# Kernel optimization log

Hardware: AMD Instinct MI355X
Metric: run time of the kernel (lower is better)

Reference implementation:

```python
import jax, jax.numpy as jnp
import numpy as np

N = 100_000      # nodes
E = 1_600_000    # edges
F_IN = 128       # input features
H = 128          # hidden features
G = 500          # graphs in batch
C = 10           # output classes


def setup_inputs() -> dict:
    key = jax.random.key(0)
    ks = jax.random.split(key, 10)
    x = jax.random.normal(ks[0], (N, F_IN), dtype=jnp.float32)
    edge_index = jax.random.randint(ks[1], (2, E), 0, N, dtype=jnp.int32)
    batch = jnp.sort(jax.random.randint(ks[2], (N,), 0, G, dtype=jnp.int32))
    s1 = 1.0 / np.sqrt(F_IN)
    s2 = 1.0 / np.sqrt(H)
    s3 = 1.0 / np.sqrt(2 * H)
    W1 = jax.random.normal(ks[3], (F_IN, H), jnp.float32) * s1
    W2 = jax.random.normal(ks[4], (H, H), jnp.float32) * s2
    W3 = jax.random.normal(ks[5], (H, H), jnp.float32) * s2
    fc_W = jax.random.normal(ks[6], (2 * H, C), jnp.float32) * s3
    return {
        "x": x, "edge_index": edge_index, "batch": batch,
        "W1": W1, "b1": jnp.zeros((H,), jnp.float32),
        "W2": W2, "b2": jnp.zeros((H,), jnp.float32),
        "W3": W3, "b3": jnp.zeros((H,), jnp.float32),
        "fc_W": fc_W, "fc_b": jnp.zeros((C,), jnp.float32),
    }


def gcn_conv(x, W, b, src, dst, dinv):
    # PyG GCNConv: add self-loops, symmetric norm deg^-1/2 * deg^-1/2,
    # transform then gather-scale-scatter aggregate at dst.
    h = x @ W                                   # [N, H]
    norm = dinv[src] * dinv[dst]                # [E]
    agg = jax.ops.segment_sum(h[src] * norm[:, None], dst, num_segments=N)
    agg = agg + h * (dinv * dinv)[:, None]      # self-loop contribution
    return agg + b


def reference(x, edge_index, batch, W1, b1, W2, b2, W3, b3, fc_W, fc_b):
    src, dst = edge_index[0], edge_index[1]
    # degree (with self-loop) from target counts, as in PyG's gcn_norm
    deg = jax.ops.segment_sum(jnp.ones((E,), x.dtype), dst, num_segments=N) + 1.0
    dinv = jax.lax.rsqrt(deg)

    h = jax.nn.relu(gcn_conv(x, W1, b1, src, dst, dinv))
    h = jax.nn.relu(gcn_conv(h, W2, b2, src, dst, dinv))
    # dropout is identity in eval mode
    h = jax.nn.relu(gcn_conv(h, W3, b3, src, dst, dinv))

    counts = jax.ops.segment_sum(jnp.ones((N,), h.dtype), batch, num_segments=G)
    x_mean = jax.ops.segment_sum(h, batch, num_segments=G) / jnp.maximum(counts, 1.0)[:, None]
    x_max = jax.ops.segment_max(h, batch, num_segments=G)
    pooled = jnp.concatenate([x_mean, x_max], axis=1)   # [G, 2H]
    return pooled @ fc_W + fc_b                          # [G, C]
```

## Files before the change

### kernel.cpp

```cpp
#include <hip/hip_runtime.h>
#include <hip/hip_fp16.h>


typedef _Float16 f16;
typedef f16 f16x8 __attribute__((ext_vector_type(8)));
typedef f16 f16x4 __attribute__((ext_vector_type(4)));
typedef f16 f16x2 __attribute__((ext_vector_type(2)));
typedef float f32x4 __attribute__((ext_vector_type(4)));

#define BIN_BITS 8
#define BINSZ 256
#define CB 256
#define SRC_BITS 17

__global__ __launch_bounds__(256) void prep_count(const float* __restrict__ W1,
                                                  const float* __restrict__ W2,
                                                  const float* __restrict__ W3,
                                                  f16x8* __restrict__ wf,
                                                  const int* __restrict__ dst,
                                                  int* __restrict__ bcnt,
                                                  int ne, int nb, int chunk) {
    int bid = blockIdx.x;
    int t = threadIdx.x;
    if (bid < 24) {
        int layer = bid >> 3;
        const float* W = (layer == 0) ? W1 : (layer == 1 ? W2 : W3);
        int tid2 = (bid & 7) * 256 + t;
        int ch = tid2 >> 10;
        int ct = (tid2 >> 8) & 3;
        int tt = (tid2 >> 6) & 3;
        int l  = tid2 & 63;
        int c  = ch * 64 + ct * 16 + (l & 15);
        int k0 = tt * 32 + ((l >> 4) << 3);
        f16x8 v;
#pragma unroll
        for (int j = 0; j < 8; ++j) v[j] = (f16)W[(size_t)(k0 + j) * 128 + c];
        wf[layer * 2048 + tid2] = v;
        return;
    }
    __shared__ int h[512];
    int b = bid - 24;
    for (int i = t; i < 512; i += 256) h[i] = 0;
    __syncthreads();
    int e0 = b * chunk, e1 = min(ne, e0 + chunk);
    for (int e = e0 + t; e < e1; e += 256)
        atomicAdd(&h[dst[e] >> BIN_BITS], 1);
    __syncthreads();
    for (int i = t; i < nb; i += 256) bcnt[(size_t)b * 512 + i] = h[i];
}

__global__ __launch_bounds__(256) void binscan(int* __restrict__ bcnt,
                                               int* __restrict__ tot, int nb) {
    __shared__ int ws[4];
    int bin = blockIdx.x;
    int t = threadIdx.x;
    int v = bcnt[(size_t)t * 512 + bin];
    int lane = t & 63, wid = t >> 6;
    int sc = v;
#pragma unroll
    for (int off = 1; off < 64; off <<= 1) {
        int u = __shfl_up(sc, off, 64);
        if (lane >= off) sc += u;
    }
    if (lane == 63) ws[wid] = sc;
    __syncthreads();
    if (t == 0) { int r = 0; for (int i = 0; i < 4; ++i) { int x = ws[i]; ws[i] = r; r += x; } }
    __syncthreads();
    int excl = ws[wid] + sc - v;
    bcnt[(size_t)t * 512 + bin] = excl;
    if (t == 255) tot[bin] = excl + v;
}

__global__ __launch_bounds__(512) void s512scan(const int* __restrict__ tot,
                                                int* __restrict__ base,
                                                int* __restrict__ row_ptr,
                                                int nb, int n, int ne) {
    __shared__ int ws[8];
    int t = threadIdx.x;
    int v = (t < nb) ? tot[t] : 0;
    int lane = t & 63, wid = t >> 6;
    int sc = v;
#pragma unroll
    for (int off = 1; off < 64; off <<= 1) {
        int u = __shfl_up(sc, off, 64);
        if (lane >= off) sc += u;
    }
    if (lane == 63) ws[wid] = sc;
    __syncthreads();
    if (t == 0) { int r = 0; for (int i = 0; i < 8; ++i) { int x = ws[i]; ws[i] = r; r += x; } }
    __syncthreads();
    int excl = ws[wid] + sc - v;
    if (t < nb) base[t] = excl;
    if (t == 0) { base[nb] = ne; row_ptr[n] = ne; }
}

__global__ __launch_bounds__(256) void bucket_place(const int* __restrict__ src,
                                                    const int* __restrict__ dst,
                                                    const int* __restrict__ base,
                                                    const int* __restrict__ bcnt,
                                                    unsigned* __restrict__ ebuf,
                                                    int ne, int nb, int chunk) {
    __shared__ int cur[512];
    __shared__ int rel[512];
    int b = blockIdx.x;
    int t = threadIdx.x;
    for (int i = t; i < 512; i += 256) {
        cur[i] = 0;
        rel[i] = (i < nb) ? (base[i] + bcnt[(size_t)b * 512 + i]) : 0;
    }
    __syncthreads();
    int e0 = b * chunk, e1 = min(ne, e0 + chunk);
    for (int e = e0 + t; e < e1; e += 256) {
        int d = dst[e];
        int s = src[e];
        int bin = d >> BIN_BITS;
        int rank = atomicAdd(&cur[bin], 1);
        ebuf[(size_t)rel[bin] + rank] = (unsigned)s | ((unsigned)(d & (BINSZ - 1)) << SRC_BITS);
    }
}

__global__ __launch_bounds__(256) void place_kernel(const unsigned* __restrict__ ebuf,
                                                    const int* __restrict__ base,
                                                    int* __restrict__ row_ptr,
                                                    int* __restrict__ csr,
                                                    float* __restrict__ dinv, int n) {
    __shared__ int hist[BINSZ];
    __shared__ int cur[BINSZ];
    __shared__ int ws[4];
    int bin = blockIdx.x;
    int t = threadIdx.x;
    int node0 = bin << BIN_BITS;
    int ebeg = base[bin], eend = base[bin + 1];
    hist[t] = 0;
    __syncthreads();
    for (int p = ebeg + t; p < eend; p += 256)
        atomicAdd(&hist[ebuf[p] >> SRC_BITS], 1);
    __syncthreads();
    int c = hist[t];
    int lane = t & 63, wid = t >> 6;
    int sc = c;
#pragma unroll
    for (int off = 1; off < 64; off <<= 1) {
        int u = __shfl_up(sc, off, 64);
        if (lane >= off) sc += u;
    }
    if (lane == 63) ws[wid] = sc;
    __syncthreads();
    if (t == 0) { int r = 0; for (int i = 0; i < 4; ++i) { int x = ws[i]; ws[i] = r; r += x; } }
    __syncthreads();
    int excl = ws[wid] + sc - c;
    int node = node0 + t;
    if (node < n) {
        row_ptr[node] = ebeg + excl;
        dinv[node] = 1.0f / sqrtf((float)c + 1.0f);
    }
    cur[t] = excl;
    __syncthreads();
    for (int p = ebeg + t; p < eend; p += 256) {
        unsigned v = ebuf[p];
        int local = v >> SRC_BITS;
        int r = atomicAdd(&cur[local], 1);
        csr[ebeg + r] = (int)(v & ((1u << SRC_BITS) - 1));
    }
}

template <bool XHALF>
__device__ __forceinline__ void gemm_core(const void* __restrict__ Xv,
                                          const f16x8* __restrict__ wf,
                                          const float* __restrict__ dinv,
                                          f16* __restrict__ Y, int n, int bid) {
    const int tid = threadIdx.x;
    const int l = tid & 63;
    const int w = tid >> 6;
    const int ch = w & 1;
    const int row0 = bid * 64 + (w >> 1) * 32;
    const int m = l & 15;
    const int kg = l >> 4;

    f16x8 bw[4][4];
#pragma unroll
    for (int ct = 0; ct < 4; ++ct)
#pragma unroll
        for (int t = 0; t < 4; ++t)
            bw[ct][t] = wf[((ch * 4 + ct) * 4 + t) * 64 + l];

    f32x4 acc[2][4];
#pragma unroll
    for (int mt = 0; mt < 2; ++mt)
#pragma unroll
        for (int ct = 0; ct < 4; ++ct) acc[mt][ct] = (f32x4){0.f, 0.f, 0.f, 0.f};

    int mrow[2];
#pragma unroll
    for (int mt = 0; mt < 2; ++mt) {
        int r = row0 + mt * 16 + m;
        mrow[mt] = (r < n) ? r : (n - 1);
    }

#pragma unroll
    for (int t = 0; t < 4; ++t) {
        f16x8 xf[2];
#pragma unroll
        for (int mt = 0; mt < 2; ++mt) {
            if constexpr (XHALF) {
                xf[mt] = *(const f16x8*)((const f16*)Xv + (size_t)mrow[mt] * 128 + t * 32 + kg * 8);
            } else {
                const float* Xf = (const float*)Xv + (size_t)mrow[mt] * 128 + t * 32 + kg * 8;
                float4 p = *(const float4*)Xf;
                float4 q = *(const float4*)(Xf + 4);
                f16x8 h;
                h[0] = (f16)p.x; h[1] = (f16)p.y; h[2] = (f16)p.z; h[3] = (f16)p.w;
                h[4] = (f16)q.x; h[5] = (f16)q.y; h[6] = (f16)q.z; h[7] = (f16)q.w;
                xf[mt] = h;
            }
        }
#pragma unroll
        for (int mt = 0; mt < 2; ++mt)
#pragma unroll
            for (int ct = 0; ct < 4; ++ct)
                acc[mt][ct] = __builtin_amdgcn_mfma_f32_16x16x32_f16(
                    bw[ct][t], xf[mt], acc[mt][ct], 0, 0, 0);
    }

#pragma unroll
    for (int mt = 0; mt < 2; ++mt) {
        int row = row0 + mt * 16 + m;
        if (row >= n) continue;
        float dv = dinv[row];
#pragma unroll
        for (int ct = 0; ct < 4; ++ct) {
            f16x4 o;
#pragma unroll
            for (int r = 0; r < 4; ++r) o[r] = (f16)(acc[mt][ct][r] * dv);
            *(f16x4*)&Y[(size_t)row * 128 + ch * 64 + ct * 16 + kg * 4] = o;
        }
    }
}

__global__ __launch_bounds__(256) void gemm_mfma_h(const f16* __restrict__ X,
                                                   const f16x8* __restrict__ wf,
                                                   const float* __restrict__ dinv,
                                                   f16* __restrict__ Y, int n) {
    gemm_core<true>(X, wf, dinv, Y, n, blockIdx.x);
}

__global__ __launch_bounds__(256) void gemm_mfma_f(const float* __restrict__ X,
                                                   const f16x8* __restrict__ wf,
                                                   const float* __restrict__ dinv,
                                                   f16* __restrict__ Y, int n) {
    gemm_core<false>(X, wf, dinv, Y, n, blockIdx.x);
}

__global__ __launch_bounds__(256) void agg_fused(const f16* __restrict__ Y,
                                                 const int* __restrict__ row_ptr,
                                                 const int* __restrict__ csr,
                                                 const float* __restrict__ dinv,
                                                 const float* __restrict__ b,
                                                 f16* __restrict__ A, int n) {
    int node = (int)((blockIdx.x * 256 + threadIdx.x) >> 6);
    node = __builtin_amdgcn_readfirstlane(node);
    if (node >= n) return;
    int lane = threadIdx.x & 63;
    const f16x2* Yv = (const f16x2*)Y;
    size_t rowOff = (size_t)node * 64;
    f16x2 sv = Yv[rowOff + lane];
    float ax = (float)sv[0], ay = (float)sv[1];
    int beg = row_ptr[node], end = row_ptr[node + 1];
    for (int e = beg; e < end; e += 8) {
        int idx[8];
        float w[8];
#pragma unroll
        for (int u = 0; u < 8; ++u) {
            int ee = e + u;
            bool live = ee < end;
            int cl = live ? ee : end - 1;
            int s = csr[cl];
            idx[u] = __builtin_amdgcn_readfirstlane(live ? s : node);
            w[u] = live ? 1.f : 0.f;
        }
#pragma unroll
        for (int u = 0; u < 8; ++u) {
            f16x2 v = Yv[(size_t)idx[u] * 64 + lane];
            ax = fmaf(w[u], (float)v[0], ax);
            ay = fmaf(w[u], (float)v[1], ay);
        }
    }
    float dn = dinv[node];
    float2 bb = *(const float2*)&b[2 * lane];
    f16x2 o;
    o[0] = (f16)fmaxf(fmaf(ax, dn, bb.x), 0.f);
    o[1] = (f16)fmaxf(fmaf(ay, dn, bb.y), 0.f);
    *((f16x2*)A + rowOff + lane) = o;
}

__device__ __forceinline__ int lower_bound(const int* __restrict__ a, int n, int key) {
    int lo = 0, hi = n;
    while (lo < hi) {
        int mid = (lo + hi) >> 1;
        if (a[mid] < key) lo = mid + 1; else hi = mid;
    }
    return lo;
}

__global__ __launch_bounds__(256) void pool_kernel(const f16* __restrict__ H,
                                                   const int* __restrict__ batch,
                                                   float* __restrict__ pooled, int n) {
    __shared__ float red[3][64][4];
    int g = blockIdx.x;
    int beg = lower_bound(batch, n, g);
    int end = lower_bound(batch, n, g + 1);
    int t = threadIdx.x, sub = t >> 6, lane = t & 63;
    const f16x2* Hv = (const f16x2*)H;
    float sx = 0.f, sy = 0.f, mx = -INFINITY, my = -INFINITY;
    for (int i = beg + sub; i < end; i += 4) {
        f16x2 v = Hv[(size_t)i * 64 + lane];
        float a = (float)v[0], c = (float)v[1];
        sx += a; sy += c;
        mx = fmaxf(mx, a); my = fmaxf(my, c);
    }
    if (sub) {
        red[sub - 1][lane][0] = sx; red[sub - 1][lane][1] = sy;
        red[sub - 1][lane][2] = mx; red[sub - 1][lane][3] = my;
    }
    __syncthreads();
    if (sub == 0) {
#pragma unroll
        for (int k = 0; k < 3; ++k) {
            sx += red[k][lane][0]; sy += red[k][lane][1];
            mx = fmaxf(mx, red[k][lane][2]); my = fmaxf(my, red[k][lane][3]);
        }
        float cnt = fmaxf((float)(end - beg), 1.0f);
        pooled[(size_t)g * 256 + 2 * lane]       = sx / cnt;
        pooled[(size_t)g * 256 + 2 * lane + 1]   = sy / cnt;
        pooled[(size_t)g * 256 + 128 + 2 * lane]     = mx;
        pooled[(size_t)g * 256 + 128 + 2 * lane + 1] = my;
    }
}

__global__ __launch_bounds__(64) void fc_kernel(const float* __restrict__ pooled,
                                                const float* __restrict__ fcW,
                                                const float* __restrict__ fcb,
                                                float* __restrict__ out, int C) {
    int g = blockIdx.x;
    __shared__ float p[256];
    int t = threadIdx.x;
    for (int k = t; k < 256; k += 64) p[k] = pooled[(size_t)g * 256 + k];
    __syncthreads();
    if (t < C) {
        float acc = fcb[t];
        for (int k = 0; k < 256; ++k) acc = fmaf(p[k], fcW[k * C + t], acc);
        out[(size_t)g * C + t] = acc;
    }
}

extern "C" void kernel_launch(void* const* d_in, const int* in_sizes, int n_in,
                              void* d_out, int out_size, void* d_ws, size_t ws_size,
                              hipStream_t stream) {
    const float* x     = (const float*)d_in[0];
    const int*   ei    = (const int*)d_in[1];
    const int*   batch = (const int*)d_in[2];
    const float* W1    = (const float*)d_in[3];
    const float* b1    = (const float*)d_in[4];
    const float* W2    = (const float*)d_in[5];
    const float* b2    = (const float*)d_in[6];
    const float* W3    = (const float*)d_in[7];
    const float* b3    = (const float*)d_in[8];
    const float* fcW   = (const float*)d_in[9];
    const float* fcb   = (const float*)d_in[10];

    const int N = in_sizes[0] / 128;
    const int E = in_sizes[1] / 2;
    const int C = in_sizes[10];
    const int G = out_size / C;
    const int NB = (N + BINSZ - 1) >> BIN_BITS;
    const int chunk = (E + CB - 1) / CB;
    float* out = (float*)d_out;

    f16*      Yh      = (f16*)d_ws;
    f16*      Ah      = Yh + (size_t)N * 128;
    f16x8*    wf      = (f16x8*)(Ah + (size_t)N * 128);
    float*    dinv    = (float*)(wf + 3 * 2048);
    float*    pooled  = dinv + N;
    int*      row_ptr = (int*)(pooled + (size_t)G * 256);
    int*      csr_src = row_ptr + N + 8;
    unsigned* ebuf    = (unsigned*)(csr_src + E);
    int*      bcnt    = (int*)(ebuf + E);
    int*      tot     = bcnt + 256 * 512;
    int*      base    = tot + 512;

    const int* src = ei;
    const int* dst = ei + E;

    prep_count<<<24 + CB, 256, 0, stream>>>(W1, W2, W3, wf, dst, bcnt, E, NB, chunk);
    binscan<<<NB, 256, 0, stream>>>(bcnt, tot, NB);
    s512scan<<<1, 512, 0, stream>>>(tot, base, row_ptr, NB, N, E);
    bucket_place<<<CB, 256, 0, stream>>>(src, dst, base, bcnt, ebuf, E, NB, chunk);
    place_kernel<<<NB, 256, 0, stream>>>(ebuf, base, row_ptr, csr_src, dinv, N);

    const int gemmBlocks = (N + 63) / 64;
    const int aggBlocks = (int)(((long long)N * 64 + 255) / 256);

    gemm_mfma_f<<<gemmBlocks, 256, 0, stream>>>(x, wf, dinv, Yh, N);
    agg_fused<<<aggBlocks, 256, 0, stream>>>(Yh, row_ptr, csr_src, dinv, b1, Ah, N);
    gemm_mfma_h<<<gemmBlocks, 256, 0, stream>>>(Ah, wf + 2048, dinv, Yh, N);
    agg_fused<<<aggBlocks, 256, 0, stream>>>(Yh, row_ptr, csr_src, dinv, b2, Ah, N);
    gemm_mfma_h<<<gemmBlocks, 256, 0, stream>>>(Ah, wf + 4096, dinv, Yh, N);
    agg_fused<<<aggBlocks, 256, 0, stream>>>(Yh, row_ptr, csr_src, dinv, b3, Ah, N);

    pool_kernel<<<G, 256, 0, stream>>>(Ah, batch, pooled, N);
    fc_kernel<<<G, 64, 0, stream>>>(pooled, fcW, fcb, out, C);
}
```

Baseline: 325.3 us.

## Fuse first-layer GEMM into degree counting and merge pooling with FC

The first-layer GEMM no longer needs dinv, so it runs without scaling inside the same launch as the destination histogram, overlapping with CSR construction. The first aggregation instead gathers dinv[src] for each edge and applies it as the edge weight. Weight packing moves to its own small kernel, and pooling and the final FC merge into one kernel, which drops the pooled buffer and one launch. The cost is an extra random dinv load per edge in layer one and the added wpack launch.

New measurement: 341.9 us. 5.1% more time.

```diff
diff --git a/kernel.cpp b/kernel.cpp
--- a/kernel.cpp
+++ b/kernel.cpp
@@ -13,158 +13,28 @@
 #define CB 256
 #define SRC_BITS 17
 
-__global__ __launch_bounds__(256) void prep_count(const float* __restrict__ W1,
-                                                  const float* __restrict__ W2,
-                                                  const float* __restrict__ W3,
-                                                  f16x8* __restrict__ wf,
-                                                  const int* __restrict__ dst,
-                                                  int* __restrict__ bcnt,
-                                                  int ne, int nb, int chunk) {
+__global__ __launch_bounds__(256) void wpack_kernel(const float* __restrict__ W1,
+                                                    const float* __restrict__ W2,
+                                                    const float* __restrict__ W3,
+                                                    f16x8* __restrict__ wf) {
     int bid = blockIdx.x;
     int t = threadIdx.x;
-    if (bid < 24) {
-        int layer = bid >> 3;
-        const float* W = (layer == 0) ? W1 : (layer == 1 ? W2 : W3);
-        int tid2 = (bid & 7) * 256 + t;
-        int ch = tid2 >> 10;
-        int ct = (tid2 >> 8) & 3;
-        int tt = (tid2 >> 6) & 3;
-        int l  = tid2 & 63;
-        int c  = ch * 64 + ct * 16 + (l & 15);
-        int k0 = tt * 32 + ((l >> 4) << 3);
-        f16x8 v;
-#pragma unroll
-        for (int j = 0; j < 8; ++j) v[j] = (f16)W[(size_t)(k0 + j) * 128 + c];
-        wf[layer * 2048 + tid2] = v;
-        return;
-    }
-    __shared__ int h[512];
-    int b = bid - 24;
-    for (int i = t; i < 512; i += 256) h[i] = 0;
-    __syncthreads();
-    int e0 = b * chunk, e1 = min(ne, e0 + chunk);
-    for (int e = e0 + t; e < e1; e += 256)
-        atomicAdd(&h[dst[e] >> BIN_BITS], 1);
-    __syncthreads();
-    for (int i = t; i < nb; i += 256) bcnt[(size_t)b * 512 + i] = h[i];
-}
-
-__global__ __launch_bounds__(256) void binscan(int* __restrict__ bcnt,
-                                               int* __restrict__ tot, int nb) {
-    __shared__ int ws[4];
-    int bin = blockIdx.x;
-    int t = threadIdx.x;
-    int v = bcnt[(size_t)t * 512 + bin];
-    int lane = t & 63, wid = t >> 6;
-    int sc = v;
-#pragma unroll
-    for (int off = 1; off < 64; off <<= 1) {
-        int u = __shfl_up(sc, off, 64);
-        if (lane >= off) sc += u;
-    }
-    if (lane == 63) ws[wid] = sc;
-    __syncthreads();
-    if (t == 0) { int r = 0; for (int i = 0; i < 4; ++i) { int x = ws[i]; ws[i] = r; r += x; } }
-    __syncthreads();
-    int excl = ws[wid] + sc - v;
-    bcnt[(size_t)t * 512 + bin] = excl;
-    if (t == 255) tot[bin] = excl + v;
-}
-
-__global__ __launch_bounds__(512) void s512scan(const int* __restrict__ tot,
-                                                int* __restrict__ base,
-                                                int* __restrict__ row_ptr,
-                                                int nb, int n, int ne) {
-    __shared__ int ws[8];
-    int t = threadIdx.x;
-    int v = (t < nb) ? tot[t] : 0;
-    int lane = t & 63, wid = t >> 6;
-    int sc = v;
-#pragma unroll
-    for (int off = 1; off < 64; off <<= 1) {
-        int u = __shfl_up(sc, off, 64);
-        if (lane >= off) sc += u;
-    }
-    if (lane == 63) ws[wid] = sc;
-    __syncthreads();
-    if (t == 0) { int r = 0; for (int i = 0; i < 8; ++i) { int x = ws[i]; ws[i] = r; r += x; } }
-    __syncthreads();
-    int excl = ws[wid] + sc - v;
-    if (t < nb) base[t] = excl;
-    if (t == 0) { base[nb] = ne; row_ptr[n] = ne; }
-}
-
-__global__ __launch_bounds__(256) void bucket_place(const int* __restrict__ src,
-                                                    const int* __restrict__ dst,
-                                                    const int* __restrict__ base,
-                                                    const int* __restrict__ bcnt,
-                                                    unsigned* __restrict__ ebuf,
-                                                    int ne, int nb, int chunk) {
-    __shared__ int cur[512];
-    __shared__ int rel[512];
-    int b = blockIdx.x;
-    int t = threadIdx.x;
-    for (int i = t; i < 512; i += 256) {
-        cur[i] = 0;
-        rel[i] = (i < nb) ? (base[i] + bcnt[(size_t)b * 512 + i]) : 0;
-    }
-    __syncthreads();
-    int e0 = b * chunk, e1 = min(ne, e0 + chunk);
-    for (int e = e0 + t; e < e1; e += 256) {
-        int d = dst[e];
-        int s = src[e];
-        int bin = d >> BIN_BITS;
-        int rank = atomicAdd(&cur[bin], 1);
-        ebuf[(size_t)rel[bin] + rank] = (unsigned)s | ((unsigned)(d & (BINSZ - 1)) << SRC_BITS);
-    }
-}
-
-__global__ __launch_bounds__(256) void place_kernel(const unsigned* __restrict__ ebuf,
-                                                    const int* __restrict__ base,
-                                                    int* __restrict__ row_ptr,
-                                                    int* __restrict__ csr,
-                                                    float* __restrict__ dinv, int n) {
-    __shared__ int hist[BINSZ];
-    __shared__ int cur[BINSZ];
-    __shared__ int ws[4];
-    int bin = blockIdx.x;
-    int t = threadIdx.x;
-    int node0 = bin << BIN_BITS;
-    int ebeg = base[bin], eend = base[bin + 1];
-    hist[t] = 0;
-    __syncthreads();
-    for (int p = ebeg + t; p < eend; p += 256)
-        atomicAdd(&hist[ebuf[p] >> SRC_BITS], 1);
-    __syncthreads();
-    int c = hist[t];
-    int lane = t & 63, wid = t >> 6;
-    int sc = c;
-#pragma unroll
-    for (int off = 1; off < 64; off <<= 1) {
-        int u = __shfl_up(sc, off, 64);
-        if (lane >= off) sc += u;
-    }
-    if (lane == 63) ws[wid] = sc;
-    __syncthreads();
-    if (t == 0) { int r = 0; for (int i = 0; i < 4; ++i) { int x = ws[i]; ws[i] = r; r += x; } }
-    __syncthreads();
-    int excl = ws[wid] + sc - c;
-    int node = node0 + t;
-    if (node < n) {
-        row_ptr[node] = ebeg + excl;
-        dinv[node] = 1.0f / sqrtf((float)c + 1.0f);
-    }
-    cur[t] = excl;
-    __syncthreads();
-    for (int p = ebeg + t; p < eend; p += 256) {
-        unsigned v = ebuf[p];
-        int local = v >> SRC_BITS;
-        int r = atomicAdd(&cur[local], 1);
-        csr[ebeg + r] = (int)(v & ((1u << SRC_BITS) - 1));
-    }
-}
-
-template <bool XHALF>
+    int layer = bid >> 3;
+    const float* W = (layer == 0) ? W1 : (layer == 1 ? W2 : W3);
+    int tid2 = (bid & 7) * 256 + t;
+    int ch = tid2 >> 10;
+    int ct = (tid2 >> 8) & 3;
+    int tt = (tid2 >> 6) & 3;
+    int l  = tid2 & 63;
+    int c  = ch * 64 + ct * 16 + (l & 15);
+    int k0 = tt * 32 + ((l >> 4) << 3);
+    f16x8 v;
+#pragma unroll
+    for (int j = 0; j < 8; ++j) v[j] = (f16)W[(size_t)(k0 + j) * 128 + c];
+    wf[layer * 2048 + tid2] = v;
+}
+
+template <bool XHALF, bool SCALE>
 __device__ __forceinline__ void gemm_core(const void* __restrict__ Xv,
                                           const f16x8* __restrict__ wf,
                                           const float* __restrict__ dinv,
@@ -226,7 +96,8 @@
     for (int mt = 0; mt < 2; ++mt) {
         int row = row0 + mt * 16 + m;
         if (row >= n) continue;
-        float dv = dinv[row];
+        float dv;
+        if constexpr (SCALE) dv = dinv[row]; else dv = 1.0f;
 #pragma unroll
         for (int ct = 0; ct < 4; ++ct) {
             f16x4 o;
@@ -234,6 +105,144 @@
             for (int r = 0; r < 4; ++r) o[r] = (f16)(acc[mt][ct][r] * dv);
             *(f16x4*)&Y[(size_t)row * 128 + ch * 64 + ct * 16 + kg * 4] = o;
         }
+    }
+}
+
+__global__ __launch_bounds__(256) void prep_fused(const int* __restrict__ dst,
+                                                  int* __restrict__ bcnt,
+                                                  const f16x8* __restrict__ wf,
+                                                  const float* __restrict__ x,
+                                                  f16* __restrict__ Y,
+                                                  int ne, int nb, int chunk, int n) {
+    int bid = blockIdx.x;
+    int t = threadIdx.x;
+    if (bid < CB) {
+        __shared__ int h[512];
+        int b = bid;
+        for (int i = t; i < 512; i += 256) h[i] = 0;
+        __syncthreads();
+        int e0 = b * chunk, e1 = min(ne, e0 + chunk);
+        for (int e = e0 + t; e < e1; e += 256)
+            atomicAdd(&h[dst[e] >> BIN_BITS], 1);
+        __syncthreads();
+        for (int i = t; i < nb; i += 256) bcnt[(size_t)b * 512 + i] = h[i];
+        return;
+    }
+    gemm_core<false, false>(x, wf, nullptr, Y, n, bid - CB);
+}
+
+__global__ __launch_bounds__(256) void binscan(int* __restrict__ bcnt,
+                                               int* __restrict__ tot, int nb) {
+    __shared__ int ws[4];
+    int bin = blockIdx.x;
+    int t = threadIdx.x;
+    int v = bcnt[(size_t)t * 512 + bin];
+    int lane = t & 63, wid = t >> 6;
+    int sc = v;
+#pragma unroll
+    for (int off = 1; off < 64; off <<= 1) {
+        int u = __shfl_up(sc, off, 64);
+        if (lane >= off) sc += u;
+    }
+    if (lane == 63) ws[wid] = sc;
+    __syncthreads();
+    if (t == 0) { int r = 0; for (int i = 0; i < 4; ++i) { int x = ws[i]; ws[i] = r; r += x; } }
+    __syncthreads();
+    int excl = ws[wid] + sc - v;
+    bcnt[(size_t)t * 512 + bin] = excl;
+    if (t == 255) tot[bin] = excl + v;
+}
+
+__global__ __launch_bounds__(512) void s512scan(const int* __restrict__ tot,
+                                                int* __restrict__ base,
+                                                int* __restrict__ row_ptr,
+                                                int nb, int n, int ne) {
+    __shared__ int ws[8];
+    int t = threadIdx.x;
+    int v = (t < nb) ? tot[t] : 0;
+    int lane = t & 63, wid = t >> 6;
+    int sc = v;
+#pragma unroll
+    for (int off = 1; off < 64; off <<= 1) {
+        int u = __shfl_up(sc, off, 64);
+        if (lane >= off) sc += u;
+    }
+    if (lane == 63) ws[wid] = sc;
+    __syncthreads();
+    if (t == 0) { int r = 0; for (int i = 0; i < 8; ++i) { int x = ws[i]; ws[i] = r; r += x; } }
+    __syncthreads();
+    int excl = ws[wid] + sc - v;
+    if (t < nb) base[t] = excl;
+    if (t == 0) { base[nb] = ne; row_ptr[n] = ne; }
+}
+
+__global__ __launch_bounds__(256) void bucket_place(const int* __restrict__ src,
+                                                    const int* __restrict__ dst,
+                                                    const int* __restrict__ base,
+                                                    const int* __restrict__ bcnt,
+                                                    unsigned* __restrict__ ebuf,
+                                                    int ne, int nb, int chunk) {
+    __shared__ int cur[512];
+    __shared__ int rel[512];
+    int b = blockIdx.x;
+    int t = threadIdx.x;
+    for (int i = t; i < 512; i += 256) {
+        cur[i] = 0;
+        rel[i] = (i < nb) ? (base[i] + bcnt[(size_t)b * 512 + i]) : 0;
+    }
+    __syncthreads();
+    int e0 = b * chunk, e1 = min(ne, e0 + chunk);
+    for (int e = e0 + t; e < e1; e += 256) {
+        int d = dst[e];
+        int s = src[e];
+        int bin = d >> BIN_BITS;
+        int rank = atomicAdd(&cur[bin], 1);
+        ebuf[(size_t)rel[bin] + rank] = (unsigned)s | ((unsigned)(d & (BINSZ - 1)) << SRC_BITS);
+    }
+}
+
+__global__ __launch_bounds__(256) void place_kernel(const unsigned* __restrict__ ebuf,
+                                                    const int* __restrict__ base,
+                                                    int* __restrict__ row_ptr,
+                                                    int* __restrict__ csr,
+                                                    float* __restrict__ dinv, int n) {
+    __shared__ int hist[BINSZ];
+    __shared__ int cur[BINSZ];
+    __shared__ int ws[4];
+    int bin = blockIdx.x;
+    int t = threadIdx.x;
+    int node0 = bin << BIN_BITS;
+    int ebeg = base[bin], eend = base[bin + 1];
+    hist[t] = 0;
+    __syncthreads();
+    for (int p = ebeg + t; p < eend; p += 256)
+        atomicAdd(&hist[ebuf[p] >> SRC_BITS], 1);
+    __syncthreads();
+    int c = hist[t];
+    int lane = t & 63, wid = t >> 6;
+    int sc = c;
+#pragma unroll
+    for (int off = 1; off < 64; off <<= 1) {
+        int u = __shfl_up(sc, off, 64);
+        if (lane >= off) sc += u;
+    }
+    if (lane == 63) ws[wid] = sc;
+    __syncthreads();
+    if (t == 0) { int r = 0; for (int i = 0; i < 4; ++i) { int x = ws[i]; ws[i] = r; r += x; } }
+    __syncthreads();
+    int excl = ws[wid] + sc - c;
+    int node = node0 + t;
+    if (node < n) {
+        row_ptr[node] = ebeg + excl;
+        dinv[node] = 1.0f / sqrtf((float)c + 1.0f);
+    }
+    cur[t] = excl;
+    __syncthreads();
+    for (int p = ebeg + t; p < eend; p += 256) {
+        unsigned v = ebuf[p];
+        int local = v >> SRC_BITS;
+        int r = atomicAdd(&cur[local], 1);
+        csr[ebeg + r] = (int)(v & ((1u << SRC_BITS) - 1));
     }
 }
 
@@ -241,16 +250,10 @@
                                                    const f16x8* __restrict__ wf,
                                                    const float* __restrict__ dinv,
                                                    f16* __restrict__ Y, int n) {
-    gemm_core<true>(X, wf, dinv, Y, n, blockIdx.x);
-}
-
-__global__ __launch_bounds__(256) void gemm_mfma_f(const float* __restrict__ X,
-                                                   const f16x8* __restrict__ wf,
-                                                   const float* __restrict__ dinv,
-                                                   f16* __restrict__ Y, int n) {
-    gemm_core<false>(X, wf, dinv, Y, n, blockIdx.x);
-}
-
+    gemm_core<true, true>(X, wf, dinv, Y, n, blockIdx.x);
+}
+
+template <bool SCALED>
 __global__ __launch_bounds__(256) void agg_fused(const f16* __restrict__ Y,
                                                  const int* __restrict__ row_ptr,
                                                  const int* __restrict__ csr,
@@ -263,8 +266,10 @@
     int lane = threadIdx.x & 63;
     const f16x2* Yv = (const f16x2*)Y;
     size_t rowOff = (size_t)node * 64;
+    float dn = dinv[node];
     f16x2 sv = Yv[rowOff + lane];
-    float ax = (float)sv[0], ay = (float)sv[1];
+    float selfw = SCALED ? 1.0f : dn;
+    float ax = selfw * (float)sv[0], ay = selfw * (float)sv[1];
     int beg = row_ptr[node], end = row_ptr[node + 1];
     for (int e = beg; e < end; e += 8) {
         int idx[8];
@@ -276,7 +281,11 @@
             int cl = live ? ee : end - 1;
             int s = csr[cl];
             idx[u] = __builtin_amdgcn_readfirstlane(live ? s : node);
-            w[u] = live ? 1.f : 0.f;
+            if constexpr (SCALED) {
+                w[u] = live ? 1.f : 0.f;
+            } else {
+                w[u] = live ? dinv[idx[u]] : 0.f;
+            }
         }
 #pragma unroll
         for (int u = 0; u < 8; ++u) {
@@ -285,7 +294,6 @@
             ay = fmaf(w[u], (float)v[1], ay);
         }
     }
-    float dn = dinv[node];
     float2 bb = *(const float2*)&b[2 * lane];
     f16x2 o;
     o[0] = (f16)fmaxf(fmaf(ax, dn, bb.x), 0.f);
@@ -302,10 +310,14 @@
     return lo;
 }
 
-__global__ __launch_bounds__(256) void pool_kernel(const f16* __restrict__ H,
-                                                   const int* __restrict__ batch,
-                                                   float* __restrict__ pooled, int n) {
+__global__ __launch_bounds__(256) void poolfc_kernel(const f16* __restrict__ H,
+                                                     const int* __restrict__ batch,
+                                                     const float* __restrict__ fcW,
+                                                     const float* __restrict__ fcb,
+                                                     float* __restrict__ out,
+                                                     int n, int C) {
     __shared__ float red[3][64][4];
+    __shared__ float p[256];
     int g = blockIdx.x;
     int beg = lower_bound(batch, n, g);
     int end = lower_bound(batch, n, g + 1);
@@ -330,21 +342,11 @@
             mx = fmaxf(mx, red[k][lane][2]); my = fmaxf(my, red[k][lane][3]);
         }
         float cnt = fmaxf((float)(end - beg), 1.0f);
-        pooled[(size_t)g * 256 + 2 * lane]       = sx / cnt;
-        pooled[(size_t)g * 256 + 2 * lane + 1]   = sy / cnt;
-        pooled[(size_t)g * 256 + 128 + 2 * lane]     = mx;
-        pooled[(size_t)g * 256 + 128 + 2 * lane + 1] = my;
-    }
-}
-
-__global__ __launch_bounds__(64) void fc_kernel(const float* __restrict__ pooled,
-                                                const float* __restrict__ fcW,
-                                                const float* __restrict__ fcb,
-                                                float* __restrict__ out, int C) {
-    int g = blockIdx.x;
-    __shared__ float p[256];
-    int t = threadIdx.x;
-    for (int k = t; k < 256; k += 64) p[k] = pooled[(size_t)g * 256 + k];
+        p[2 * lane]           = sx / cnt;
+        p[2 * lane + 1]       = sy / cnt;
+        p[128 + 2 * lane]     = mx;
+        p[128 + 2 * lane + 1] = my;
+    }
     __syncthreads();
     if (t < C) {
         float acc = fcb[t];
@@ -380,8 +382,7 @@
     f16*      Ah      = Yh + (size_t)N * 128;
     f16x8*    wf      = (f16x8*)(Ah + (size_t)N * 128);
     float*    dinv    = (float*)(wf + 3 * 2048);
-    float*    pooled  = dinv + N;
-    int*      row_ptr = (int*)(pooled + (size_t)G * 256);
+    int*      row_ptr = (int*)(dinv + N);
     int*      csr_src = row_ptr + N + 8;
     unsigned* ebuf    = (unsigned*)(csr_src + E);
     int*      bcnt    = (int*)(ebuf + E);
@@ -391,22 +392,21 @@
     const int* src = ei;
     const int* dst = ei + E;
 
-    prep_count<<<24 + CB, 256, 0, stream>>>(W1, W2, W3, wf, dst, bcnt, E, NB, chunk);
+    const int gemmBlocks = (N + 63) / 64;
+    const int aggBlocks = (int)(((long long)N * 64 + 255) / 256);
+
+    wpack_kernel<<<24, 256, 0, stream>>>(W1, W2, W3, wf);
+    prep_fused<<<CB + gemmBlocks, 256, 0, stream>>>(dst, bcnt, wf, x, Yh, E, NB, chunk, N);
     binscan<<<NB, 256, 0, stream>>>(bcnt, tot, NB);
     s512scan<<<1, 512, 0, stream>>>(tot, base, row_ptr, NB, N, E);
     bucket_place<<<CB, 256, 0, stream>>>(src, dst, base, bcnt, ebuf, E, NB, chunk);
     place_kernel<<<NB, 256, 0, stream>>>(ebuf, base, row_ptr, csr_src, dinv, N);
 
-    const int gemmBlocks = (N + 63) / 64;
-    const int aggBlocks = (int)(((long long)N * 64 + 255) / 256);
-
-    gemm_mfma_f<<<gemmBlocks, 256, 0, stream>>>(x, wf, dinv, Yh, N);
-    agg_fused<<<aggBlocks, 256, 0, stream>>>(Yh, row_ptr, csr_src, dinv, b1, Ah, N);
+    agg_fused<false><<<aggBlocks, 256, 0, stream>>>(Yh, row_ptr, csr_src, dinv, b1, Ah, N);
     gemm_mfma_h<<<gemmBlocks, 256, 0, stream>>>(Ah, wf + 2048, dinv, Yh, N);
-    agg_fused<<<aggBlocks, 256, 0, stream>>>(Yh, row_ptr, csr_src, dinv, b2, Ah, N);
+    agg_fused<true><<<aggBlocks, 256, 0, stream>>>(Yh, row_ptr, csr_src, dinv, b2, Ah, N);
     gemm_mfma_h<<<gemmBlocks, 256, 0, stream>>>(Ah, wf + 4096, dinv, Yh, N);
-    agg_fused<<<aggBlocks, 256, 0, stream>>>(Yh, row_ptr, csr_src, dinv, b3, Ah, N);
-
-    pool_kernel<<<G, 256, 0, stream>>>(Ah, batch, pooled, N);
-    fc_kernel<<<G, 64, 0, stream>>>(pooled, fcW, fcb, out, C);
-}
+    agg_fused<true><<<aggBlocks, 256, 0, stream>>>(Yh, row_ptr, csr_src, dinv, b3, Ah, N);
+
+    poolfc_kernel<<<G, 256, 0, stream>>>(Ah, batch, fcW, fcb, out, N, C);
+}
```
